# Performance work log

Hardware: AMD Instinct MI355X
Metric: run time of the kernel (lower is better)

Reference implementation:

```python
import jax, jax.numpy as jnp
import numpy as np

N = 8192          # num_nodes
E = 262144        # num_edges = N * avg_degree(32)
K_SIGN = 1000.0   # ExactModel k
EPSILON = 5.0     # ExactModel epsilon


def setup_inputs() -> dict:
    key = jax.random.key(0)
    k1, k2, k3, k4 = jax.random.split(key, 4)
    src = jax.random.randint(k1, (E,), 0, N)
    dst = jax.random.randint(k2, (E,), 0, N)
    edge_index = jnp.stack([src, dst]).astype(jnp.int32)          # (2, E)
    # partition vector, elements in {1, ..., N}
    p = jax.random.randint(k3, (N,), 1, N + 1).astype(jnp.float32)  # (N,)
    x = jax.random.normal(k4, (N, 1), dtype=jnp.float32)            # node features
    return {"edge_index": edge_index, "p": p, "x": x}


def reference(edge_index, p, x):
    """infoco1 (segment logsumexp over edges with self-loops) followed by one
    refine step: pairwise difference matrix + CustomSignFunction tanh + row-sum."""
    n = p.shape[0]
    log_n = jnp.log(jnp.asarray(n, dtype=p.dtype))
    loops = jnp.arange(n, dtype=edge_index.dtype)
    src = jnp.concatenate([edge_index[0], loops])   # add_self_loops
    dst = jnp.concatenate([edge_index[1], loops])
    # contributions_log = log(p_i) + p_j * log(N)
    contrib = jnp.log(p[src]) + p[dst] * log_n      # (E + N,)
    # numerically stable segment log-sum-exp over incoming edges of each node
    mx = jax.ops.segment_max(contrib, dst, num_segments=n)              # scatter_max
    se = jax.ops.segment_sum(jnp.exp(contrib - mx[dst]), dst, num_segments=n)  # scatter_add
    S = mx + jnp.log(se) + jnp.dot(x[:, 0], p)      # infoco1: S_log + <x, p>
    # refine: all-pairs sign refinement, D_1 = tanh(k * (X - X^T) - eps)
    X = S[:, None]                                   # (N, 1)
    D1 = jnp.tanh(K_SIGN * (X - X.T) - EPSILON)      # (N, N)
    return D1.sum(axis=1)                            # (N,)
```

## Files before the change

kernel.cpp:

```cpp
#include <hip/hip_runtime.h>
#include <math.h>

#define K_SIGN 1000.0f
#define EPSILON 5.0f

#define D_HI ((EPSILON + 12.0f) / K_SIGN)
#define D_LO ((EPSILON - 12.0f) / K_SIGN)

#define NB_HIST 64


__global__ void __launch_bounds__(256) k_hist(
        const int* __restrict__ src, const int* __restrict__ dst,
        const float* __restrict__ p, const float* __restrict__ x,
        int* __restrict__ Hpriv, double* __restrict__ C,
        int* __restrict__ PFX, int* __restrict__ order, int e, int n) {
    __shared__ int buf[8192];
    __shared__ int csum[256];
    __shared__ double dred[4];
    int tid = threadIdx.x;
    int b = blockIdx.x;

    int4* b4 = (int4*)buf;
    for (int i = tid; i < n / 4; i += 256) b4[i] = make_int4(0, 0, 0, 0);
    __syncthreads();

    if (b < NB_HIST) {
        int per = (e + NB_HIST - 1) / NB_HIST;
        int t0 = b * per;
        int t1 = min(t0 + per, e);
        for (int t = t0 + tid; t < t1; t += 256)
            atomicAdd(&buf[dst[t]], (int)p[src[t]]);
        __syncthreads();
        int4* o4 = (int4*)(Hpriv + b * n);
        for (int i = tid; i < n / 4; i += 256) o4[i] = b4[i];
        return;
    }

    double acc = 0.0;
    for (int i = tid; i < n; i += 256) {
        float pv = p[i];
        atomicAdd(&buf[(int)pv - 1], 1);
        acc += (double)x[i] * (double)pv;
    }
    for (int off = 32; off > 0; off >>= 1)
        acc += __shfl_down(acc, off, 64);
    if ((tid & 63) == 0) dred[tid >> 6] = acc;
    __syncthreads();
    if (tid == 0) *C = dred[0] + dred[1] + dred[2] + dred[3];

    int cw = n / 256;
    int base = tid * cw;
    int s = 0;
    for (int k = 0; k < cw; ++k) s += buf[base + k];
    csum[tid] = s;
    __syncthreads();
    for (int off = 1; off < 256; off <<= 1) {
        int v = (tid >= off) ? csum[tid - off] : 0;
        __syncthreads();
        csum[tid] += v;
        __syncthreads();
    }
    int run = (tid == 0) ? 0 : csum[tid - 1];
    for (int k = 0; k < cw; ++k) {
        int h = buf[base + k];
        PFX[base + k] = run;
        buf[base + k] = run;
        run += h;
    }
    if (tid == 0) PFX[n] = n;
    __syncthreads();

    for (int i = tid; i < n; i += 256) {
        int r = atomicAdd(&buf[(int)p[i] - 1], 1);
        order[r] = i;
    }
}

__global__ void __launch_bounds__(256) k_merge(
        const int* __restrict__ Hpriv, const float* __restrict__ p,
        const double* __restrict__ C, float* __restrict__ S,
        int n, float log_n) {
    __shared__ int part[4][64];
    int q = threadIdx.x >> 6;
    int l = threadIdx.x & 63;
    int i = blockIdx.x * 64 + l;
    int s = 0;
#pragma unroll
    for (int b = q * 16; b < q * 16 + 16; ++b) s += Hpriv[b * n + i];
    part[q][l] = s;
    __syncthreads();
    if (q == 0) {
        float pv = p[i];
        int t = (int)pv + part[0][l] + part[1][l] + part[2][l] + part[3][l];
        S[i] = (logf((float)t) + pv * log_n) + (float)(*C);
    }
}

__global__ void __launch_bounds__(64) k_out(const float* __restrict__ S,
                                            const float* __restrict__ p,
                                            const int* __restrict__ PFX,
                                            const int* __restrict__ order,
                                            float* __restrict__ out, int n) {
    int i = blockIdx.x * 64 + threadIdx.x;
    if (i >= n) return;
    int pi = (int)p[i];
    int base = PFX[pi - 1];
    int g = PFX[pi] - base;
    float si = S[i];
    float acc = (float)(base - (n - base - g));
    for (int k = 0; k < g; ++k) {
        int j = order[base + k];
        float d = si - S[j];
        if (d > D_HI) acc += 1.0f;
        else if (d < D_LO) acc -= 1.0f;
        else acc += tanhf(fmaf(K_SIGN, d, -EPSILON));
    }
    out[i] = acc;
}

extern "C" void kernel_launch(void* const* d_in, const int* in_sizes, int n_in,
                              void* d_out, int out_size, void* d_ws, size_t ws_size,
                              hipStream_t stream) {
    const int* edge_index = (const int*)d_in[0];
    const float* p = (const float*)d_in[1];
    const float* x = (const float*)d_in[2];
    float* out = (float*)d_out;

    int e = in_sizes[0] / 2;
    int n = in_sizes[1];
    const int* src = edge_index;
    const int* dst = edge_index + e;

    double* C = (double*)d_ws;
    float* S = (float*)((char*)d_ws + 16);
    int* PFX = (int*)(S + n);
    int* order = PFX + (n + 4);
    int* Hpriv = order + n;

    float log_n = logf((float)n);

    k_hist<<<NB_HIST + 1, 256, 0, stream>>>(src, dst, p, x, Hpriv, C,
                                            PFX, order, e, n);
    k_merge<<<n / 64, 256, 0, stream>>>(Hpriv, p, C, S, n, log_n);
    k_out<<<n / 64, 64, 0, stream>>>(S, p, PFX, order, out, n);
}
```

Before: 95.58 us.

## Spread edge histogram over 256 blocks with vectorized loads and LDS p cache

Raises the number of histogram blocks from 64 to 256 so each thread handles exactly four edges via int4 loads of src/dst. Each block also caches p converted to int in shared memory, so the gather of p[src] reads LDS instead of global memory. The merge kernel is reshaped to sum 256 private histograms with 8 slices of 32 lanes. The cost is four times more private histogram traffic written and read back, plus an extra 32KB of shared memory per block. The edge loop assumes e divides evenly by 1024 with no tail handling.

```diff
diff --git a/kernel.cpp b/kernel.cpp
--- a/kernel.cpp
+++ b/kernel.cpp
@@ -7,7 +7,7 @@
 #define D_HI ((EPSILON + 12.0f) / K_SIGN)
 #define D_LO ((EPSILON - 12.0f) / K_SIGN)
 
-#define NB_HIST 64
+#define NB_HIST 256
 
 
 __global__ void __launch_bounds__(256) k_hist(
@@ -16,21 +16,30 @@
         int* __restrict__ Hpriv, double* __restrict__ C,
         int* __restrict__ PFX, int* __restrict__ order, int e, int n) {
     __shared__ int buf[8192];
+    __shared__ int pl[8192];
     __shared__ int csum[256];
     __shared__ double dred[4];
     int tid = threadIdx.x;
     int b = blockIdx.x;
 
     int4* b4 = (int4*)buf;
-    for (int i = tid; i < n / 4; i += 256) b4[i] = make_int4(0, 0, 0, 0);
+    const float4* p4 = (const float4*)p;
+    int4* pl4 = (int4*)pl;
+    for (int i = tid; i < n / 4; i += 256) {
+        b4[i] = make_int4(0, 0, 0, 0);
+        float4 v = p4[i];
+        pl4[i] = make_int4((int)v.x, (int)v.y, (int)v.z, (int)v.w);
+    }
     __syncthreads();
 
     if (b < NB_HIST) {
-        int per = (e + NB_HIST - 1) / NB_HIST;
-        int t0 = b * per;
-        int t1 = min(t0 + per, e);
-        for (int t = t0 + tid; t < t1; t += 256)
-            atomicAdd(&buf[dst[t]], (int)p[src[t]]);
+        int base = b * (e / NB_HIST) + tid * 4;
+        int4 s4 = *(const int4*)(src + base);
+        int4 d4 = *(const int4*)(dst + base);
+        atomicAdd(&buf[d4.x], pl[s4.x]);
+        atomicAdd(&buf[d4.y], pl[s4.y]);
+        atomicAdd(&buf[d4.z], pl[s4.z]);
+        atomicAdd(&buf[d4.w], pl[s4.w]);
         __syncthreads();
         int4* o4 = (int4*)(Hpriv + b * n);
         for (int i = tid; i < n / 4; i += 256) o4[i] = b4[i];
@@ -81,18 +90,22 @@
         const int* __restrict__ Hpriv, const float* __restrict__ p,
         const double* __restrict__ C, float* __restrict__ S,
         int n, float log_n) {
-    __shared__ int part[4][64];
-    int q = threadIdx.x >> 6;
-    int l = threadIdx.x & 63;
-    int i = blockIdx.x * 64 + l;
+    __shared__ int part[8][32];
+    int lane = threadIdx.x & 31;
+    int slice = threadIdx.x >> 5;
+    int i = blockIdx.x * 32 + lane;
     int s = 0;
+#pragma unroll 8
+    for (int h = slice * 32; h < slice * 32 + 32; ++h)
+        s += Hpriv[h * n + i];
+    part[slice][lane] = s;
+    __syncthreads();
+    if (threadIdx.x < 32) {
+        int t = 0;
 #pragma unroll
-    for (int b = q * 16; b < q * 16 + 16; ++b) s += Hpriv[b * n + i];
-    part[q][l] = s;
-    __syncthreads();
-    if (q == 0) {
+        for (int q = 0; q < 8; ++q) t += part[q][lane];
         float pv = p[i];
-        int t = (int)pv + part[0][l] + part[1][l] + part[2][l] + part[3][l];
+        t += (int)pv;
         S[i] = (logf((float)t) + pv * log_n) + (float)(*C);
     }
 }
@@ -142,6 +155,6 @@
 
     k_hist<<<NB_HIST + 1, 256, 0, stream>>>(src, dst, p, x, Hpriv, C,
                                             PFX, order, e, n);
-    k_merge<<<n / 64, 256, 0, stream>>>(Hpriv, p, C, S, n, log_n);
+    k_merge<<<n / 32, 256, 0, stream>>>(Hpriv, p, C, S, n, log_n);
     k_out<<<n / 64, 64, 0, stream>>>(S, p, PFX, order, out, n);
 }
```

After: 101.8 us. 6.6% more time.
